# Kernel optimization log

Hardware: AMD Instinct MI355X
Metric: run time of the kernel (lower is better)

Reference implementation:

```python
import jax, jax.numpy as jnp
import numpy as np

EPS = 1e-5  # BatchNorm eps


def _add_self_loops(edge_index, num_nodes):
    loop = jnp.arange(num_nodes, dtype=edge_index.dtype)
    src = jnp.concatenate([edge_index[0], loop])
    dst = jnp.concatenate([edge_index[1], loop])
    return src, dst


def _gcn_conv(x, src, dst, norm, W, b, num_nodes):
    # PyG GCNConv: out = D^{-1/2} (A+I) D^{-1/2} (x W) + b
    h = x @ W                                # [N, out_dim]
    msg = h[src] * norm[:, None]             # [E+N, out_dim] gathered messages
    out = jax.ops.segment_sum(msg, dst, num_segments=num_nodes)
    return out + b


def _batch_norm(x, gamma, beta):
    # training-mode batch statistics over the node dimension (biased var)
    mean = jnp.mean(x, axis=0)
    var = jnp.var(x, axis=0)
    return (x - mean) * jax.lax.rsqrt(var + EPS) * gamma + beta


def setup_inputs() -> dict:
    key = jax.random.key(0)
    ks = jax.random.split(key, 10)
    N, E = 50000, 800000
    d_in, d_h, d_mid, d_out = 1536, 512, 128, 5

    x = jax.random.normal(ks[0], (N, d_in), dtype=jnp.float32)
    edge_index = jax.random.randint(ks[1], (2, E), 0, N, dtype=jnp.int32)

    def glorot(k, fan_in, fan_out):
        s = jnp.sqrt(6.0 / (fan_in + fan_out))
        return jax.random.uniform(k, (fan_in, fan_out), jnp.float32, -s, s)

    return {
        "x": x,
        "edge_index": edge_index,
        "W1": glorot(ks[2], d_in, d_h), "b1": jnp.zeros((d_h,), jnp.float32),
        "W2": glorot(ks[3], d_h, d_mid), "b2": jnp.zeros((d_mid,), jnp.float32),
        "W3": glorot(ks[4], d_mid, d_out), "b3": jnp.zeros((d_out,), jnp.float32),
        "gamma1": jnp.ones((d_h,), jnp.float32), "beta1": jnp.zeros((d_h,), jnp.float32),
        "gamma2": jnp.ones((d_mid,), jnp.float32), "beta2": jnp.zeros((d_mid,), jnp.float32),
    }


def reference(x, edge_index, W1, b1, W2, b2, W3, b3, gamma1, beta1, gamma2, beta2):
    N = x.shape[0]
    src, dst = _add_self_loops(edge_index, N)
    # symmetric degree normalization deg^{-1/2}[src] * deg^{-1/2}[dst]
    deg = jax.ops.segment_sum(jnp.ones_like(dst, dtype=x.dtype), dst, num_segments=N)
    inv_sqrt = jnp.where(deg > 0, jax.lax.rsqrt(deg), 0.0)
    norm = inv_sqrt[src] * inv_sqrt[dst]

    h = _gcn_conv(x, src, dst, norm, W1, b1, N)
    h = jax.nn.relu(_batch_norm(h, gamma1, beta1))  # dropout is identity in eval
    h = _gcn_conv(h, src, dst, norm, W2, b2, N)
    h = jax.nn.relu(_batch_norm(h, gamma2, beta2))
    h = _gcn_conv(h, src, dst, norm, W3, b3, N)
    return jax.nn.log_softmax(h, axis=1)
```

## Files before the change

### kernel.cpp

```cpp
#include <hip/hip_runtime.h>
#include <cstddef>
#include <cstdint>

typedef short s16x8 __attribute__((ext_vector_type(8)));
typedef unsigned short u16x4 __attribute__((ext_vector_type(4)));
typedef unsigned short u16x8 __attribute__((ext_vector_type(8)));
typedef float f32x4 __attribute__((ext_vector_type(4)));

__device__ __forceinline__ unsigned short f2bf(float f) {
  unsigned int u = __float_as_uint(f);
  u = (u + 0x7fffu + ((u >> 16) & 1u)) >> 16;
  return (unsigned short)u;
}
__device__ __forceinline__ float bf2f(unsigned short u) {
  return __uint_as_float(((unsigned int)u) << 16);
}

__device__ __forceinline__ void gl2lds16(const unsigned short* g, unsigned short* l) {
  __builtin_amdgcn_global_load_lds(
      (const __attribute__((address_space(1))) unsigned int*)g,
      (__attribute__((address_space(3))) unsigned int*)l, 16, 0, 0);
}
__device__ __forceinline__ void gl2lds16f(const float* g, float* l) {
  __builtin_amdgcn_global_load_lds(
      (const __attribute__((address_space(1))) unsigned int*)g,
      (__attribute__((address_space(3))) unsigned int*)l, 16, 0, 0);
}

static inline size_t alignup(size_t x) { return (x + 255) & ~(size_t)255; }

__global__ void count_kernel(const int* __restrict__ dst, int* __restrict__ counts, int E) {
  int e = blockIdx.x * blockDim.x + threadIdx.x;
  if (e < E) atomicAdd(&counts[dst[e]], 1);
}

__global__ void block_sum_kernel(const int* __restrict__ counts, int* __restrict__ bsum, int n) {
  __shared__ int red[256];
  int i = blockIdx.x * 256 + threadIdx.x;
  red[threadIdx.x] = (i < n) ? counts[i] : 0;
  __syncthreads();
  #pragma unroll
  for (int o = 128; o > 0; o >>= 1) {
    if (threadIdx.x < o) red[threadIdx.x] += red[threadIdx.x + o];
    __syncthreads();
  }
  if (threadIdx.x == 0) bsum[blockIdx.x] = red[0];
}

__global__ void scan_bsum_kernel(int* __restrict__ bsum, int nb) {
  __shared__ int s[256];
  int t = threadIdx.x;
  s[t] = (t < nb) ? bsum[t] : 0;
  __syncthreads();
  #pragma unroll
  for (int o = 1; o < 256; o <<= 1) {
    int v = (t >= o) ? s[t - o] : 0;
    __syncthreads();
    s[t] += v;
    __syncthreads();
  }
  if (t < nb) bsum[t] = (t == 0) ? 0 : s[t - 1];
}

__global__ void scan_apply_kernel(const int* __restrict__ counts, const int* __restrict__ bpre,
                                  int* __restrict__ offsets, float* __restrict__ inv_s, int n) {
  __shared__ int s[256];
  int t = threadIdx.x;
  int i = blockIdx.x * 256 + t;
  int c = (i < n) ? counts[i] : 0;
  s[t] = c;
  __syncthreads();
  #pragma unroll
  for (int o = 1; o < 256; o <<= 1) {
    int v = (t >= o) ? s[t - o] : 0;
    __syncthreads();
    s[t] += v;
    __syncthreads();
  }
  if (i < n) {
    offsets[i + 1] = s[t] + bpre[blockIdx.x];
    inv_s[i] = rsqrtf((float)(c + 1));
  }
  if (i == 0) offsets[0] = 0;
}

__global__ void fill_kernel(const int* __restrict__ src, const int* __restrict__ dst,
                            const int* __restrict__ offsets, int* __restrict__ cursor,
                            int* __restrict__ csr_src, int E) {
  int e = blockIdx.x * blockDim.x + threadIdx.x;
  if (e >= E) return;
  int d = dst[e];
  int pos = atomicAdd(&cursor[d], 1);
  csr_src[offsets[d] + pos] = src[e];
}

__global__ void transpose_both_kernel(const float* __restrict__ W1, unsigned short* __restrict__ W1t,
                                      const float* __restrict__ W2, unsigned short* __restrict__ W2t) {
  __shared__ float tile[32][33];
  int b = blockIdx.x;
  const float* W;
  unsigned short* Wt;
  int K, N, kx, ny;
  if (b < 768) { W = W1; Wt = W1t; K = 1536; N = 512; kx = b % 48; ny = b / 48; }
  else { b -= 768; W = W2; Wt = W2t; K = 512; N = 128; kx = b % 16; ny = b / 16; }
  int k0 = kx * 32, n0 = ny * 32;
  int tx = threadIdx.x & 31, ty = threadIdx.x >> 5;
  #pragma unroll
  for (int i = 0; i < 32; i += 8)
    tile[ty + i][tx] = W[(size_t)(k0 + ty + i) * N + n0 + tx];
  __syncthreads();
  #pragma unroll
  for (int i = 0; i < 32; i += 8)
    Wt[(size_t)(n0 + ty + i) * K + k0 + tx] = f2bf(tile[tx][ty + i]);
}

__global__ __launch_bounds__(512) void gemm1_kernel(
    const float* __restrict__ A, const unsigned short* __restrict__ B,
    unsigned short* __restrict__ C, int M) {
  __shared__ __align__(16) float As[2][128 * 32];
  __shared__ __align__(16) unsigned short Bs[2][256 * 32];
  const int K = 1536;
  const int NT = 48;
  int tid = threadIdx.x, lane = tid & 63, w = tid >> 6;

  int nwg = gridDim.x * gridDim.y;
  int orig = blockIdx.y * gridDim.x + blockIdx.x;
  int q = nwg >> 3, r = nwg & 7;
  int xcd = orig & 7, loc = orig >> 3;
  int wg = (xcd < r) ? xcd * (q + 1) + loc : r * (q + 1) + (xcd - r) * q + loc;
  int bx = wg & 1, by = wg >> 1;

  int m0 = by * 128, n0 = bx * 256;
  int wm = (w >> 2) * 64, wn = (w & 3) * 64;

  f32x4 acc[4][4];
  #pragma unroll
  for (int i = 0; i < 4; i++)
    #pragma unroll
    for (int j = 0; j < 4; j++) acc[i][j] = (f32x4){0.f, 0.f, 0.f, 0.f};

  int row0 = tid >> 3, slot0 = tid & 7;
  int row1 = 64 + row0;
  const float* agp0 = &A[(size_t)min(m0 + row0, M - 1) * K + ((slot0 ^ (row0 & 7)) << 2)];
  const float* agp1 = &A[(size_t)min(m0 + row1, M - 1) * K + ((slot0 ^ (row1 & 7)) << 2)];
  int adst0 = tid * 4, adst1 = (512 + tid) * 4;
  int brow = tid >> 2, bslot = tid & 3;
  int bsrc = (bslot ^ ((brow >> 1) & 3)) << 3;
  const unsigned short* bgp0 = &B[(size_t)(n0 + brow) * K + bsrc];
  const unsigned short* bgp1 = &B[(size_t)(n0 + 128 + brow) * K + bsrc];
  int bdst0 = tid * 8, bdst1 = (512 + tid) * 8;

  gl2lds16f(agp0, &As[0][adst0]);
  gl2lds16f(agp1, &As[0][adst1]);
  gl2lds16(bgp0, &Bs[0][bdst0]);
  gl2lds16(bgp1, &Bs[0][bdst1]);
  __syncthreads();

  int cur = 0;
  for (int t = 0; t < NT; t++) {
    if (t + 1 < NT) {
      int kb = (t + 1) * 32;
      gl2lds16f(agp0 + kb, &As[cur ^ 1][adst0]);
      gl2lds16f(agp1 + kb, &As[cur ^ 1][adst1]);
      gl2lds16(bgp0 + kb, &Bs[cur ^ 1][bdst0]);
      gl2lds16(bgp1 + kb, &Bs[cur ^ 1][bdst1]);
    }
    int jc = lane >> 4;
    s16x8 af[4], bfr[4];
    #pragma unroll
    for (int i = 0; i < 4; i++) {
      int rr = wm + i * 16 + (lane & 15);
      f32x4 v0 = *reinterpret_cast<const f32x4*>(&As[cur][rr * 32 + (((2 * jc) ^ (rr & 7)) << 2)]);
      f32x4 v1 = *reinterpret_cast<const f32x4*>(&As[cur][rr * 32 + (((2 * jc + 1) ^ (rr & 7)) << 2)]);
      unsigned int c0, c1, c2, c3;
      asm("v_cvt_pk_bf16_f32 %0, %1, %2" : "=v"(c0) : "v"(v0[0]), "v"(v0[1]));
      asm("v_cvt_pk_bf16_f32 %0, %1, %2" : "=v"(c1) : "v"(v0[2]), "v"(v0[3]));
      asm("v_cvt_pk_bf16_f32 %0, %1, %2" : "=v"(c2) : "v"(v1[0]), "v"(v1[1]));
      asm("v_cvt_pk_bf16_f32 %0, %1, %2" : "=v"(c3) : "v"(v1[2]), "v"(v1[3]));
      uint4 pk;
      pk.x = c0; pk.y = c1; pk.z = c2; pk.w = c3;
      af[i] = __builtin_bit_cast(s16x8, pk);
      int rn = wn + i * 16 + (lane & 15);
      bfr[i] = *reinterpret_cast<const s16x8*>(
          &Bs[cur][rn * 32 + ((jc ^ ((rn >> 1) & 3)) << 3)]);
    }
    #pragma unroll
    for (int i = 0; i < 4; i++)
      #pragma unroll
      for (int j = 0; j < 4; j++)
        acc[i][j] = __builtin_amdgcn_mfma_f32_16x16x32_bf16(af[i], bfr[j], acc[i][j], 0, 0, 0);
    __syncthreads();
    cur ^= 1;
  }

  #pragma unroll
  for (int i = 0; i < 4; i++) {
    #pragma unroll
    for (int j = 0; j < 4; j++) {
      int col = n0 + wn + j * 16 + (lane & 15);
      #pragma unroll
      for (int r2 = 0; r2 < 4; r2++) {
        int row = m0 + wm + i * 16 + (lane >> 4) * 4 + r2;
        if (row < M) C[(size_t)row * 512 + col] = f2bf(acc[i][j][r2]);
      }
    }
  }
}

#define LDT 72
__global__ __launch_bounds__(256) void gemm2_kernel(
    const unsigned short* __restrict__ A, const unsigned short* __restrict__ Bt,
    const float* __restrict__ accum, const float* __restrict__ gamma,
    const float* __restrict__ beta, unsigned short* __restrict__ C, int M, float invN) {
  const int N = 128, K = 512;
  __shared__ unsigned short As[64 * LDT];
  __shared__ unsigned short Bs[128 * LDT];
  __shared__ float scs[512], shs[512];
  int tid = threadIdx.x;
  int m0 = blockIdx.y * 64;
  int w = tid >> 6, lane = tid & 63;
  int wm = (w >> 1) * 32, wn = (w & 1) * 64;

  for (int c = tid; c < 512; c += 256) {
    float mean = accum[c] * invN;
    float var = accum[512 + c] * invN - mean * mean;
    float s = gamma[c] * rsqrtf(var + 1e-5f);
    scs[c] = s;
    shs[c] = beta[c] - mean * s;
  }
  __syncthreads();

  f32x4 acc[2][4];
  #pragma unroll
  for (int i = 0; i < 2; i++)
    #pragma unroll
    for (int j = 0; j < 4; j++) acc[i][j] = (f32x4){0.f, 0.f, 0.f, 0.f};

  for (int k0 = 0; k0 < K; k0 += 64) {
    #pragma unroll
    for (int r = 0; r < 2; r++) {
      int idx = r * 256 + tid;
      int row = idx >> 3;
      int seg = (idx & 7) * 8;
      int gr = m0 + row;
      u16x8 v = (u16x8){0, 0, 0, 0, 0, 0, 0, 0};
      if (gr < M) v = *reinterpret_cast<const u16x8*>(&A[(size_t)gr * K + k0 + seg]);
      int c = k0 + seg;
      u16x8 p;
      #pragma unroll
      for (int j = 0; j < 8; j++) {
        float f = fmaxf(bf2f(v[j]) * scs[c + j] + shs[c + j], 0.f);
        p[j] = f2bf(f);
      }
      *reinterpret_cast<u16x8*>(&As[row * LDT + seg]) = p;
    }
    #pragma unroll
    for (int r = 0; r < 4; r++) {
      int idx = r * 256 + tid;
      int n = idx >> 3;
      int seg = (idx & 7) * 8;
      u16x8 v = *reinterpret_cast<const u16x8*>(&Bt[(size_t)n * K + k0 + seg]);
      *reinterpret_cast<u16x8*>(&Bs[n * LDT + seg]) = v;
    }
    __syncthreads();
    #pragma unroll
    for (int ks = 0; ks < 2; ks++) {
      s16x8 af[2], bfr[4];
      #pragma unroll
      for (int i = 0; i < 2; i++)
        af[i] = *reinterpret_cast<const s16x8*>(
            &As[(wm + i * 16 + (lane & 15)) * LDT + ks * 32 + (lane >> 4) * 8]);
      #pragma unroll
      for (int j = 0; j < 4; j++)
        bfr[j] = *reinterpret_cast<const s16x8*>(
            &Bs[(wn + j * 16 + (lane & 15)) * LDT + ks * 32 + (lane >> 4) * 8]);
      #pragma unroll
      for (int i = 0; i < 2; i++)
        #pragma unroll
        for (int j = 0; j < 4; j++)
          acc[i][j] = __builtin_amdgcn_mfma_f32_16x16x32_bf16(af[i], bfr[j], acc[i][j], 0, 0, 0);
    }
    __syncthreads();
  }
  #pragma unroll
  for (int i = 0; i < 2; i++) {
    #pragma unroll
    for (int j = 0; j < 4; j++) {
      int col = wn + j * 16 + (lane & 15);
      #pragma unroll
      for (int r = 0; r < 4; r++) {
        int row = m0 + wm + i * 16 + (lane >> 4) * 4 + r;
        if (row < M) C[(size_t)row * N + col] = f2bf(acc[i][j][r]);
      }
    }
  }
}

__global__ void agg512_kernel(const unsigned short* __restrict__ h, const int* __restrict__ offsets,
                              const int* __restrict__ csr, const float* __restrict__ inv_s,
                              unsigned short* __restrict__ out, float* __restrict__ accum, int n) {
  __shared__ float rs[512], rq[512];
  int wv = threadIdx.x >> 6, lane = threadIdx.x & 63;
  for (int c = threadIdx.x; c < 512; c += 256) { rs[c] = 0.f; rq[c] = 0.f; }
  __syncthreads();
  const u16x8* h8 = reinterpret_cast<const u16x8*>(h);
  float s[8], qsum[8];
  #pragma unroll
  for (int j = 0; j < 8; j++) { s[j] = 0.f; qsum[j] = 0.f; }
  for (int i = 0; i < 8; i++) {
    int node = blockIdx.x * 32 + wv * 8 + i;
    if (node >= n) break;
    float di = inv_s[node];
    size_t rb = (size_t)node * 64;
    float acc[8];
    u16x8 v0 = h8[rb + lane];
    float dd = di * di;
    #pragma unroll
    for (int j = 0; j < 8; j++) acc[j] = bf2f(v0[j]) * dd;
    int e = offsets[node], e1 = offsets[node + 1];
    for (; e + 7 < e1; e += 8) {
      int si[8];
      float wi[8];
      u16x8 vi[8];
      #pragma unroll
      for (int k = 0; k < 8; k++) si[k] = csr[e + k];
      #pragma unroll
      for (int k = 0; k < 8; k++) wi[k] = inv_s[si[k]] * di;
      #pragma unroll
      for (int k = 0; k < 8; k++) vi[k] = h8[(size_t)si[k] * 64 + lane];
      #pragma unroll
      for (int j = 0; j < 8; j++) {
        float a = acc[j];
        #pragma unroll
        for (int k = 0; k < 8; k++) a += bf2f(vi[k][j]) * wi[k];
        acc[j] = a;
      }
    }
    for (; e < e1; e++) {
      int sA = csr[e];
      float wA = inv_s[sA] * di;
      u16x8 vA = h8[(size_t)sA * 64 + lane];
      #pragma unroll
      for (int j = 0; j < 8; j++) acc[j] += bf2f(vA[j]) * wA;
    }
    u16x8 o;
    #pragma unroll
    for (int j = 0; j < 8; j++) {
      unsigned short b = f2bf(acc[j]);
      o[j] = b;
      float gv = bf2f(b);
      s[j] += gv;
      qsum[j] += gv * gv;
    }
    reinterpret_cast<u16x8*>(out)[rb + lane] = o;
  }
  #pragma unroll
  for (int j = 0; j < 8; j++) {
    atomicAdd(&rs[lane * 8 + j], s[j]);
    atomicAdd(&rq[lane * 8 + j], qsum[j]);
  }
  __syncthreads();
  for (int c = threadIdx.x; c < 512; c += 256) {
    atomicAdd(&accum[c], rs[c]);
    atomicAdd(&accum[512 + c], rq[c]);
  }
}

__global__ void agg128_kernel(const unsigned short* __restrict__ h, const int* __restrict__ offsets,
                              const int* __restrict__ csr, const float* __restrict__ inv_s,
                              unsigned short* __restrict__ out, float* __restrict__ accum, int n) {
  __shared__ float rs[128], rq[128];
  int wv = threadIdx.x >> 6, lane = threadIdx.x & 63;
  if (threadIdx.x < 128) { rs[threadIdx.x] = 0.f; rq[threadIdx.x] = 0.f; }
  __syncthreads();
  const unsigned int* h2 = reinterpret_cast<const unsigned int*>(h);
  float s0 = 0.f, q0 = 0.f, s1 = 0.f, q1 = 0.f;
  for (int i = 0; i < 8; i++) {
    int node = blockIdx.x * 32 + wv * 8 + i;
    if (node >= n) break;
    float di = inv_s[node];
    size_t rb = (size_t)node * 64;
    unsigned int u0 = h2[rb + lane];
    float dd = di * di;
    float alo = __uint_as_float(u0 << 16) * dd;
    float ahi = __uint_as_float(u0 & 0xffff0000u) * dd;
    int e = offsets[node], e1 = offsets[node + 1];
    for (; e + 7 < e1; e += 8) {
      int si[8];
      float wi[8];
      unsigned int ui[8];
      #pragma unroll
      for (int k = 0; k < 8; k++) si[k] = csr[e + k];
      #pragma unroll
      for (int k = 0; k < 8; k++) wi[k] = inv_s[si[k]] * di;
      #pragma unroll
      for (int k = 0; k < 8; k++) ui[k] = h2[(size_t)si[k] * 64 + lane];
      #pragma unroll
      for (int k = 0; k < 8; k++) {
        alo += __uint_as_float(ui[k] << 16) * wi[k];
        ahi += __uint_as_float(ui[k] & 0xffff0000u) * wi[k];
      }
    }
    for (; e < e1; e++) {
      int sA = csr[e];
      float wA = inv_s[sA] * di;
      unsigned int uA = h2[(size_t)sA * 64 + lane];
      alo += __uint_as_float(uA << 16) * wA;
      ahi += __uint_as_float(uA & 0xffff0000u) * wA;
    }
    unsigned short blo = f2bf(alo), bhi = f2bf(ahi);
    unsigned int uo = ((unsigned int)bhi << 16) | (unsigned int)blo;
    reinterpret_cast<unsigned int*>(out)[rb + lane] = uo;
    float glo = bf2f(blo), ghi = bf2f(bhi);
    s0 += glo; q0 += glo * glo; s1 += ghi; q1 += ghi * ghi;
  }
  atomicAdd(&rs[2 * lane], s0);
  atomicAdd(&rq[2 * lane], q0);
  atomicAdd(&rs[2 * lane + 1], s1);
  atomicAdd(&rq[2 * lane + 1], q1);
  __syncthreads();
  if (threadIdx.x < 128) {
    atomicAdd(&accum[threadIdx.x], rs[threadIdx.x]);
    atomicAdd(&accum[128 + threadIdx.x], rq[threadIdx.x]);
  }
}

__global__ void gemm3_kernel(const unsigned short* __restrict__ A, const float* __restrict__ W,
                             const float* __restrict__ accum, const float* __restrict__ gamma,
                             const float* __restrict__ beta, float* __restrict__ C, int M,
                             float invN) {
  __shared__ float Ws[128 * 5];
  __shared__ float scs[128], shs[128];
  int tid = threadIdx.x;
  for (int i = tid; i < 128 * 5; i += blockDim.x) Ws[i] = W[i];
  if (tid < 128) {
    float mean = accum[tid] * invN;
    float var = accum[128 + tid] * invN - mean * mean;
    float s = gamma[tid] * rsqrtf(var + 1e-5f);
    scs[tid] = s;
    shs[tid] = beta[tid] - mean * s;
  }
  __syncthreads();
  int row = blockIdx.x * blockDim.x + tid;
  if (row >= M) return;
  float acc[5] = {0.f, 0.f, 0.f, 0.f, 0.f};
  const u16x8* a8 = reinterpret_cast<const u16x8*>(A + (size_t)row * 128);
  for (int k8 = 0; k8 < 16; k8++) {
    u16x8 v = a8[k8];
    int k = k8 * 8;
    #pragma unroll
    for (int j = 0; j < 8; j++) {
      float f = fmaxf(bf2f(v[j]) * scs[k + j] + shs[k + j], 0.f);
      #pragma unroll
      for (int c = 0; c < 5; c++) acc[c] += f * Ws[(k + j) * 5 + c];
    }
  }
  #pragma unroll
  for (int j = 0; j < 5; j++) C[(size_t)row * 5 + j] = acc[j];
}

__global__ void agg3_lsm_kernel(const float* __restrict__ h, const int* __restrict__ offsets,
                                const int* __restrict__ csr, const float* __restrict__ inv_s,
                                const float* __restrict__ b3, float* __restrict__ out, int n) {
  int node = blockIdx.x * blockDim.x + threadIdx.x;
  if (node >= n) return;
  float di = inv_s[node];
  float acc[5];
  #pragma unroll
  for (int j = 0; j < 5; j++) acc[j] = h[(size_t)node * 5 + j] * di * di;
  int s0 = offsets[node], s1 = offsets[node + 1];
  for (int e = s0; e < s1; e++) {
    int s = csr[e];
    float wgt = inv_s[s] * di;
    #pragma unroll
    for (int j = 0; j < 5; j++) acc[j] += h[(size_t)s * 5 + j] * wgt;
  }
  #pragma unroll
  for (int j = 0; j < 5; j++) acc[j] += b3[j];
  float m = acc[0];
  #pragma unroll
  for (int j = 1; j < 5; j++) m = fmaxf(m, acc[j]);
  float sum = 0.f;
  #pragma unroll
  for (int j = 0; j < 5; j++) sum += expf(acc[j] - m);
  float lse = logf(sum);
  #pragma unroll
  for (int j = 0; j < 5; j++) out[(size_t)node * 5 + j] = acc[j] - m - lse;
}

extern "C" void kernel_launch(void* const* d_in, const int* in_sizes, int n_in,
                              void* d_out, int out_size, void* d_ws, size_t ws_size,
                              hipStream_t stream) {
  const float* x      = (const float*)d_in[0];
  const int*   ei     = (const int*)d_in[1];
  const float* W1     = (const float*)d_in[2];
  const float* b3     = (const float*)d_in[7];
  const float* W2     = (const float*)d_in[4];
  const float* W3     = (const float*)d_in[6];
  const float* gamma1 = (const float*)d_in[8];
  const float* beta1  = (const float*)d_in[9];
  const float* gamma2 = (const float*)d_in[10];
  const float* beta2  = (const float*)d_in[11];

  const int N = in_sizes[0] / 1536;
  const int E = in_sizes[1] / 2;
  const int* src = ei;
  const int* dst = ei + E;

  const int mblocks = (N + 127) / 128;
  const int Mpad = mblocks * 128;
  const int nb = (N + 255) / 256;

  char* ws = (char*)d_ws;
  size_t szRA = alignup((size_t)N * 512 * sizeof(float));
  size_t szXB = alignup((size_t)Mpad * 1536 * sizeof(unsigned short));
  char* RAb = ws;
  char* RBb = ws + szRA;
  char* sp = ws + szRA + szXB;
  char* zbase = sp;
  int* counts    = (int*)sp;          sp += alignup((size_t)N * 4);
  int* cursor    = (int*)sp;          sp += alignup((size_t)N * 4);
  float* accumA  = (float*)sp;        sp += alignup(1024 * 4);
  float* accumB  = (float*)sp;        sp += alignup(256 * 4);
  size_t zspan = (size_t)(sp - zbase);
  int* offsets  = (int*)sp;           sp += alignup((size_t)(N + 1) * 4);
  int* csr_src  = (int*)sp;           sp += alignup((size_t)E * 4);
  float* inv_s  = (float*)sp;         sp += alignup((size_t)N * 4);
  unsigned short* W1t = (unsigned short*)sp; sp += alignup((size_t)512 * 1536 * 2);
  unsigned short* W2t = (unsigned short*)sp; sp += alignup((size_t)128 * 512 * 2);
  int* bsum     = (int*)sp;           sp += alignup(256 * 4);

  unsigned short* H1  = (unsigned short*)RAb;
  unsigned short* G1  = (unsigned short*)RBb;
  unsigned short* H2  = (unsigned short*)RAb;
  unsigned short* G2  = (unsigned short*)RBb;
  float*          H3  = (float*)RAb;

  hipMemsetAsync(zbase, 0, zspan, stream);

  count_kernel<<<(E + 255) / 256, 256, 0, stream>>>(dst, counts, E);
  block_sum_kernel<<<nb, 256, 0, stream>>>(counts, bsum, N);
  scan_bsum_kernel<<<1, 256, 0, stream>>>(bsum, nb);
  scan_apply_kernel<<<nb, 256, 0, stream>>>(counts, bsum, offsets, inv_s, N);
  fill_kernel<<<(E + 255) / 256, 256, 0, stream>>>(src, dst, offsets, cursor, csr_src, E);

  transpose_both_kernel<<<832, 256, 0, stream>>>(W1, W1t, W2, W2t);

  int aggblocks32 = (N + 31) / 32;
  float invN = 1.0f / N;

  gemm1_kernel<<<dim3(2, mblocks), 512, 0, stream>>>(x, W1t, H1, N);
  agg512_kernel<<<aggblocks32, 256, 0, stream>>>(H1, offsets, csr_src, inv_s, G1, accumA, N);

  gemm2_kernel<<<dim3(1, (N + 63) / 64), 256, 0, stream>>>(G1, W2t, accumA, gamma1, beta1, H2, N,
                                                           invN);
  agg128_kernel<<<aggblocks32, 256, 0, stream>>>(H2, offsets, csr_src, inv_s, G2, accumB, N);

  gemm3_kernel<<<(N + 255) / 256, 256, 0, stream>>>(G2, W3, accumB, gamma2, beta2, H3, N, invN);
  agg3_lsm_kernel<<<(N + 255) / 256, 256, 0, stream>>>(H3, offsets, csr_src, inv_s, b3,
                                                       (float*)d_out, N);
}
```

Before: 558.8 us.

## Double-buffer gemm2 with async B loads and XOR-swizzled LDS tiles

Rewrites the second GEMM (fused BN+ReLU on A) to double-buffer its LDS tiles. The weight tile is loaded with global_load_lds, and the next A tile is prefetched into registers while MFMAs run on the current buffer. The padded LDS layout is replaced by an XOR swizzle to avoid bank conflicts, and one barrier per k-step is dropped. In exchange it uses more LDS and holds more registers for the prefetched values, which may reduce occupancy.

```diff
diff --git a/kernel.cpp b/kernel.cpp
--- a/kernel.cpp
+++ b/kernel.cpp
@@ -207,17 +207,17 @@
   }
 }
 
-#define LDT 72
 __global__ __launch_bounds__(256) void gemm2_kernel(
     const unsigned short* __restrict__ A, const unsigned short* __restrict__ Bt,
     const float* __restrict__ accum, const float* __restrict__ gamma,
     const float* __restrict__ beta, unsigned short* __restrict__ C, int M, float invN) {
-  const int N = 128, K = 512;
-  __shared__ unsigned short As[64 * LDT];
-  __shared__ unsigned short Bs[128 * LDT];
+  const int K = 512;
+  const int NT = 8;
+  __shared__ __align__(16) unsigned short As[2][64 * 64];
+  __shared__ __align__(16) unsigned short Bs[2][128 * 64];
   __shared__ float scs[512], shs[512];
   int tid = threadIdx.x;
-  int m0 = blockIdx.y * 64;
+  int m0 = blockIdx.x * 64;
   int w = tid >> 6, lane = tid & 63;
   int wm = (w >> 1) * 32, wn = (w & 1) * 64;
 
@@ -236,52 +236,84 @@
     #pragma unroll
     for (int j = 0; j < 4; j++) acc[i][j] = (f32x4){0.f, 0.f, 0.f, 0.f};
 
-  for (int k0 = 0; k0 < K; k0 += 64) {
-    #pragma unroll
-    for (int r = 0; r < 2; r++) {
-      int idx = r * 256 + tid;
-      int row = idx >> 3;
-      int seg = (idx & 7) * 8;
-      int gr = m0 + row;
-      u16x8 v = (u16x8){0, 0, 0, 0, 0, 0, 0, 0};
-      if (gr < M) v = *reinterpret_cast<const u16x8*>(&A[(size_t)gr * K + k0 + seg]);
-      int c = k0 + seg;
-      u16x8 p;
-      #pragma unroll
-      for (int j = 0; j < 8; j++) {
-        float f = fmaxf(bf2f(v[j]) * scs[c + j] + shs[c + j], 0.f);
-        p[j] = f2bf(f);
+  int arow = tid >> 3, aslot = tid & 7;
+  int ac0 = aslot * 8;
+  int adst0 = arow * 64 + ((aslot ^ (arow & 7)) << 3);
+  int adst1 = (arow + 32) * 64 + ((aslot ^ ((arow + 32) & 7)) << 3);
+  bool aok0 = (m0 + arow) < M, aok1 = (m0 + arow + 32) < M;
+  const unsigned short* agp0 = &A[(size_t)(m0 + arow) * K + ac0];
+  const unsigned short* agp1 = &A[(size_t)(m0 + arow + 32) * K + ac0];
+  const unsigned short* bgp[4];
+  int bdst[4];
+  #pragma unroll
+  for (int p = 0; p < 4; p++) {
+    int idx = p * 256 + tid;
+    int row = idx >> 3, slot = idx & 7;
+    bgp[p] = &Bt[(size_t)row * K + ((slot ^ (row & 7)) << 3)];
+    bdst[p] = idx * 8;
+  }
+
+  auto bn_write = [&](unsigned short* AsW, int kb, u16x8 v0, u16x8 v1) {
+    u16x8 p0, p1;
+    int c0 = kb + ac0;
+    #pragma unroll
+    for (int j = 0; j < 8; j++) {
+      p0[j] = f2bf(fmaxf(bf2f(v0[j]) * scs[c0 + j] + shs[c0 + j], 0.f));
+      p1[j] = f2bf(fmaxf(bf2f(v1[j]) * scs[c0 + j] + shs[c0 + j], 0.f));
+    }
+    *reinterpret_cast<u16x8*>(&AsW[adst0]) = p0;
+    *reinterpret_cast<u16x8*>(&AsW[adst1]) = p1;
+  };
+  auto load_a = [&](int kb, u16x8& v0, u16x8& v1) {
+    v0 = (u16x8){0, 0, 0, 0, 0, 0, 0, 0};
+    v1 = (u16x8){0, 0, 0, 0, 0, 0, 0, 0};
+    if (aok0) v0 = *reinterpret_cast<const u16x8*>(agp0 + kb);
+    if (aok1) v1 = *reinterpret_cast<const u16x8*>(agp1 + kb);
+  };
+
+  #pragma unroll
+  for (int p = 0; p < 4; p++) gl2lds16(bgp[p], &Bs[0][bdst[p]]);
+  {
+    u16x8 v0, v1;
+    load_a(0, v0, v1);
+    bn_write(As[0], 0, v0, v1);
+  }
+  __syncthreads();
+
+  int cur = 0;
+  for (int t = 0; t < NT; t++) {
+    u16x8 n0r, n1r;
+    if (t + 1 < NT) {
+      int kb = (t + 1) * 64;
+      #pragma unroll
+      for (int p = 0; p < 4; p++) gl2lds16(bgp[p] + kb, &Bs[cur ^ 1][bdst[p]]);
+      load_a(kb, n0r, n1r);
+    }
+    #pragma unroll
+    for (int ks = 0; ks < 2; ks++) {
+      int s = ks * 4 + (lane >> 4);
+      s16x8 af[2], bfr[4];
+      #pragma unroll
+      for (int i = 0; i < 2; i++) {
+        int ra = wm + i * 16 + (lane & 15);
+        af[i] = *reinterpret_cast<const s16x8*>(&As[cur][ra * 64 + ((s ^ (ra & 7)) << 3)]);
       }
-      *reinterpret_cast<u16x8*>(&As[row * LDT + seg]) = p;
-    }
-    #pragma unroll
-    for (int r = 0; r < 4; r++) {
-      int idx = r * 256 + tid;
-      int n = idx >> 3;
-      int seg = (idx & 7) * 8;
-      u16x8 v = *reinterpret_cast<const u16x8*>(&Bt[(size_t)n * K + k0 + seg]);
-      *reinterpret_cast<u16x8*>(&Bs[n * LDT + seg]) = v;
-    }
-    __syncthreads();
-    #pragma unroll
-    for (int ks = 0; ks < 2; ks++) {
-      s16x8 af[2], bfr[4];
-      #pragma unroll
-      for (int i = 0; i < 2; i++)
-        af[i] = *reinterpret_cast<const s16x8*>(
-            &As[(wm + i * 16 + (lane & 15)) * LDT + ks * 32 + (lane >> 4) * 8]);
-      #pragma unroll
-      for (int j = 0; j < 4; j++)
-        bfr[j] = *reinterpret_cast<const s16x8*>(
-            &Bs[(wn + j * 16 + (lane & 15)) * LDT + ks * 32 + (lane >> 4) * 8]);
+      #pragma unroll
+      for (int j = 0; j < 4; j++) {
+        int rb = wn + j * 16 + (lane & 15);
+        bfr[j] = *reinterpret_cast<const s16x8*>(&Bs[cur][rb * 64 + ((s ^ (rb & 7)) << 3)]);
+      }
       #pragma unroll
       for (int i = 0; i < 2; i++)
         #pragma unroll
         for (int j = 0; j < 4; j++)
           acc[i][j] = __builtin_amdgcn_mfma_f32_16x16x32_bf16(af[i], bfr[j], acc[i][j], 0, 0, 0);
     }
-    __syncthreads();
-  }
+    if (t + 1 < NT) bn_write(As[cur ^ 1], (t + 1) * 64, n0r, n1r);
+    __syncthreads();
+    cur ^= 1;
+  }
+
   #pragma unroll
   for (int i = 0; i < 2; i++) {
     #pragma unroll
@@ -290,7 +322,7 @@
       #pragma unroll
       for (int r = 0; r < 4; r++) {
         int row = m0 + wm + i * 16 + (lane >> 4) * 4 + r;
-        if (row < M) C[(size_t)row * N + col] = f2bf(acc[i][j][r]);
+        if (row < M) C[(size_t)row * 128 + col] = f2bf(acc[i][j][r]);
       }
     }
   }
@@ -552,8 +584,7 @@
   gemm1_kernel<<<dim3(2, mblocks), 512, 0, stream>>>(x, W1t, H1, N);
   agg512_kernel<<<aggblocks32, 256, 0, stream>>>(H1, offsets, csr_src, inv_s, G1, accumA, N);
 
-  gemm2_kernel<<<dim3(1, (N + 63) / 64), 256, 0, stream>>>(G1, W2t, accumA, gamma1, beta1, H2, N,
-                                                           invN);
+  gemm2_kernel<<<(N + 63) / 64, 256, 0, stream>>>(G1, W2t, accumA, gamma1, beta1, H2, N, invN);
   agg128_kernel<<<aggblocks32, 256, 0, stream>>>(H2, offsets, csr_src, inv_s, G2, accumB, N);
 
   gemm3_kernel<<<(N + 255) / 256, 256, 0, stream>>>(G2, W3, accumB, gamma2, beta2, H3, N, invN);
```

New measurement: 556.9 us (median of 2 runs). About the same (-0.3%).
